# Performance work log

Hardware: AMD Instinct MI355X
Metric: run time of the kernel (lower is better)

Reference implementation:

```python
import jax, jax.numpy as jnp
import numpy as np

EPS = 1e-7
CP_NUM = 16
P_NUM_TOTAL = 1024
P_PER_SEG = P_NUM_TOTAL // CP_NUM  # 64, matches int(p_num / cp_num)
ALPHA = 0.5


def setup_inputs() -> dict:
    key = jax.random.key(0)
    cps = jax.random.normal(key, (16384, CP_NUM, 2), dtype=jnp.float32)
    return {"cps": cps}


def reference(cps):
    # Centripetal Catmull-Rom spline sampling (closed curve), fully vectorized
    # over segments and sample points instead of the original double Python loop.
    B, S, D = cps.shape  # S == cp_num
    P = P_PER_SEG

    # Close the curve: append first control point.  [B, S+1, D]
    cc = jnp.concatenate([cps, cps[:, :1, :]], axis=1)

    # Boundary extension lengths (detached in the original via .detach_()).
    l01 = jax.lax.stop_gradient(
        jnp.sqrt(jnp.sum((cc[:, 0] - cc[:, 1]) ** 2, axis=-1) + EPS))[:, None]
    llast = jax.lax.stop_gradient(
        jnp.sqrt(jnp.sum((cc[:, -1] - cc[:, -2]) ** 2, axis=-1) + EPS))[:, None]
    aux_first = cc[:, 0] - l01 / llast * (cc[:, -1] - cc[:, -2])
    aux_last = cc[:, -1] + llast / l01 * (cc[:, 1] - cc[:, 0])
    # Auxiliary control points. [B, S+3, D]
    aux = jnp.concatenate([aux_first[:, None], cc, aux_last[:, None]], axis=1)

    # Centripetal knot vector: t[i] = t[i-1] + ||aux_i - aux_{i-1}||^alpha (detached).
    seg_len = jnp.sqrt(jnp.sum((aux[:, 1:] - aux[:, :-1]) ** 2, axis=-1)) ** ALPHA
    t = jnp.concatenate(
        [jnp.zeros((B, 1), dtype=cps.dtype), jnp.cumsum(seg_len, axis=1)], axis=1)
    t = jax.lax.stop_gradient(t)  # [B, S+3]

    idx = jnp.arange(S)
    # Knot windows per segment, broadcast to [B, S, 1, 1].
    t0 = t[:, idx][:, :, None, None]
    t1 = t[:, idx + 1][:, :, None, None]
    t2 = t[:, idx + 2][:, :, None, None]
    t3 = t[:, idx + 3][:, :, None, None]
    # Control point windows per segment, broadcast to [B, S, 1, D].
    P0 = aux[:, idx][:, :, None, :]
    P1 = aux[:, idx + 1][:, :, None, :]
    P2 = aux[:, idx + 2][:, :, None, :]
    P3 = aux[:, idx + 3][:, :, None, :]

    # batch_linspace(t1, t2, P): P points inclusive of both endpoints. [B,S,P,1]
    u = jnp.linspace(0.0, 1.0, P, dtype=cps.dtype)[None, None, :, None]
    tv = t1 + (t2 - t1) * u

    # Barry-Goldman pyramid of weighted blends.
    x01 = (t1 - tv) / (t1 - t0) * P0 + (tv - t0) / (t1 - t0) * P1
    x12 = (t2 - tv) / (t2 - t1) * P1 + (tv - t1) / (t2 - t1) * P2
    x23 = (t3 - tv) / (t3 - t2) * P2 + (tv - t2) / (t3 - t2) * P3
    x012 = (t2 - tv) / (t2 - t0) * x01 + (tv - t0) / (t2 - t0) * x12
    x123 = (t3 - tv) / (t3 - t1) * x12 + (tv - t1) / (t3 - t1) * x23
    pts = (t2 - tv) / (t2 - t1) * x012 + (tv - t1) / (t2 - t1) * x123  # [B,S,P,D]

    return pts.reshape(B, S * P, D)
```

## Files before the change

kernel.cpp:

```cpp
#include <hip/hip_runtime.h>

#define CP_NUM 16
#define SEGS   16
#define WPB    4
#define BLK    (WPB * 64)

typedef float f32x4 __attribute__((ext_vector_type(4)));

__device__ __forceinline__ float frcp(float x) { return __builtin_amdgcn_rcpf(x); }

__global__ __launch_bounds__(BLK, 8) void spline_poly_kernel(
    const float* __restrict__ cps, float* __restrict__ out, int nb)
{
    __shared__ __align__(16) float s_cp [WPB][CP_NUM * 2];
    __shared__ __align__(16) float s_aux[WPB][19 * 2];
    __shared__ __align__(16) float s_t  [WPB][20];
    __shared__ __align__(16) float s_seg[WPB][SEGS][12];

    const int lane = threadIdx.x & 63;
    const int wv   = threadIdx.x >> 6;
    const int b    = blockIdx.x * WPB + wv;
    if (b >= nb) return;

    if (lane < 8) {
        reinterpret_cast<float4*>(s_cp[wv])[lane] =
            reinterpret_cast<const float4*>(cps + (size_t)b * (CP_NUM * 2))[lane];
    }
    __builtin_amdgcn_wave_barrier();

    if (lane < 19) {
        const float c0x = s_cp[wv][0],  c0y = s_cp[wv][1];
        const float c1x = s_cp[wv][2],  c1y = s_cp[wv][3];
        const float cLx = s_cp[wv][30], cLy = s_cp[wv][31];
        const float dx01 = c0x - c1x, dy01 = c0y - c1y;
        const float l01   = sqrtf(dx01 * dx01 + dy01 * dy01 + 1e-7f);
        const float dxl = c0x - cLx, dyl = c0y - cLy;
        const float llast = sqrtf(dxl * dxl + dyl * dyl + 1e-7f);
        float ax, ay;
        if (lane == 0) {
            const float r = l01 * frcp(llast);
            ax = c0x - r * dxl;  ay = c0y - r * dyl;
        } else if (lane <= CP_NUM) {
            ax = s_cp[wv][(lane - 1) * 2];  ay = s_cp[wv][(lane - 1) * 2 + 1];
        } else if (lane == CP_NUM + 1) {
            ax = c0x;  ay = c0y;
        } else {
            const float r = llast * frcp(l01);
            ax = c0x + r * (c1x - c0x);  ay = c0y + r * (c1y - c0y);
        }
        s_aux[wv][lane * 2]     = ax;
        s_aux[wv][lane * 2 + 1] = ay;
    }
    __builtin_amdgcn_wave_barrier();

    float len = 0.f;
    if (lane < 18) {
        const float dx = s_aux[wv][(lane + 1) * 2]     - s_aux[wv][lane * 2];
        const float dy = s_aux[wv][(lane + 1) * 2 + 1] - s_aux[wv][lane * 2 + 1];
        len = sqrtf(sqrtf(dx * dx + dy * dy));
    }
    #pragma unroll
    for (int d = 1; d < 32; d <<= 1) {
        const float n = __shfl_up(len, d);
        if (lane >= d) len += n;
    }
    if (lane == 0) s_t[wv][0] = 0.f;
    if (lane < 18) s_t[wv][lane + 1] = len;
    __builtin_amdgcn_wave_barrier();

    if (lane < SEGS) {
        const float t0 = s_t[wv][lane];
        const float t1 = s_t[wv][lane + 1];
        const float t2 = s_t[wv][lane + 2];
        const float t3 = s_t[wv][lane + 3];
        const float A  = t1 - t0, Bk = t2 - t1, C = t3 - t2;
        const float BC = Bk + C;
        const float r10 = frcp(A);
        const float r21 = frcp(Bk);
        const float r32 = frcp(C);
        const float r20 = frcp(A + Bk);
        const float r31 = frcp(BC);

        float* sp = s_seg[wv][lane];
        #pragma unroll
        for (int d = 0; d < 2; ++d) {
            const float P0 = s_aux[wv][lane * 2 + d];
            const float P1 = s_aux[wv][lane * 2 + 2 + d];
            const float P2 = s_aux[wv][lane * 2 + 4 + d];
            const float P3 = s_aux[wv][lane * 2 + 6 + d];
            const float L1c0 = P1,                        L1c1 = (P1 - P0) * r10;
            const float L2c0 = P1,                        L2c1 = (P2 - P1) * r21;
            const float L3c0 = (BC * P2 - Bk * P3) * r32, L3c1 = (P3 - P2) * r32;
            const float Q1c0 = r20 * (Bk * L1c0 + A * L2c0);
            const float Q1c1 = r20 * (Bk * L1c1 - L1c0 + A * L2c1 + L2c0);
            const float Q1c2 = r20 * (L2c1 - L1c1);
            const float Q2c0 = r31 * (BC * L2c0);
            const float Q2c1 = r31 * (BC * L2c1 - L2c0 + L3c0);
            const float Q2c2 = r31 * (L3c1 - L2c1);
            sp[d * 4 + 0] = Q1c0;
            sp[d * 4 + 1] = Q1c1 + r21 * (Q2c0 - Q1c0);
            sp[d * 4 + 2] = Q1c2 + r21 * (Q2c1 - Q1c1);
            sp[d * 4 + 3] = r21 * (Q2c2 - Q1c2);
        }
        sp[8] = Bk;
    }
    __builtin_amdgcn_wave_barrier();

    f32x4* outw = reinterpret_cast<f32x4*>(out + (size_t)b * (SEGS * 64 * 2));
    const int   hi = lane >> 5;
    const float q0 = (float)((lane & 31) * 2)     * (1.f / 63.f);
    const float q1 = (float)((lane & 31) * 2 + 1) * (1.f / 63.f);
    #pragma unroll
    for (int i = 0; i < 8; ++i) {
        const float* sp = s_seg[wv][2 * i + hi];
        const f32x4 cx = *reinterpret_cast<const f32x4*>(sp);
        const f32x4 cy = *reinterpret_cast<const f32x4*>(sp + 4);
        const float dt = sp[8];
        const float s0 = dt * q0;
        const float s1 = dt * q1;
        f32x4 o;
        o.x = ((cx.w * s0 + cx.z) * s0 + cx.y) * s0 + cx.x;
        o.y = ((cy.w * s0 + cy.z) * s0 + cy.y) * s0 + cy.x;
        o.z = ((cx.w * s1 + cx.z) * s1 + cx.y) * s1 + cx.x;
        o.w = ((cy.w * s1 + cy.z) * s1 + cy.y) * s1 + cy.x;
        outw[lane + 64 * i] = o;
    }
}

extern "C" void kernel_launch(void* const* d_in, const int* in_sizes, int n_in,
                              void* d_out, int out_size, void* d_ws, size_t ws_size,
                              hipStream_t stream) {
    const float* cps = (const float*)d_in[0];
    float* out = (float*)d_out;
    const int B = in_sizes[0] / (CP_NUM * 2);
    const int grid = (B + WPB - 1) / WPB;
    spline_poly_kernel<<<grid, BLK, 0, stream>>>(cps, out, B);
}
```

Baseline: 27.88 us.

## Process two curves per wavefront using half-wave setup lanes

Each wavefront now handles two batch items. Each 32-lane half computes the auxiliary points, the knot prefix sum (via 32-wide shuffles) and the segment polynomial coefficients for one curve, then the whole wave writes both curves' outputs. The goal is to fill the mostly idle lanes in the serial setup phase and halve the grid size, trading that for a longer output loop per wave and less parallelism across waves.

```diff
diff --git a/kernel.cpp b/kernel.cpp
--- a/kernel.cpp
+++ b/kernel.cpp
@@ -12,67 +12,73 @@
 __global__ __launch_bounds__(BLK, 8) void spline_poly_kernel(
     const float* __restrict__ cps, float* __restrict__ out, int nb)
 {
-    __shared__ __align__(16) float s_cp [WPB][CP_NUM * 2];
-    __shared__ __align__(16) float s_aux[WPB][19 * 2];
-    __shared__ __align__(16) float s_t  [WPB][20];
-    __shared__ __align__(16) float s_seg[WPB][SEGS][12];
+    __shared__ __align__(16) float4 s_cp [WPB][16];
+    __shared__ __align__(16) float  s_aux[WPB][2][19 * 2];
+    __shared__ __align__(16) float  s_t  [WPB][2][20];
+    __shared__ __align__(16) float  s_seg[WPB][2][SEGS][12];
 
     const int lane = threadIdx.x & 63;
     const int wv   = threadIdx.x >> 6;
-    const int b    = blockIdx.x * WPB + wv;
-    if (b >= nb) return;
+    const int half = lane >> 5;
+    const int r    = lane & 31;
+    const int pw   = blockIdx.x * WPB + wv;
+    const int base = pw * 2;
+    if (base >= nb) return;
+    const int ncur = (nb - base < 2) ? (nb - base) : 2;
 
-    if (lane < 8) {
-        reinterpret_cast<float4*>(s_cp[wv])[lane] =
-            reinterpret_cast<const float4*>(cps + (size_t)b * (CP_NUM * 2))[lane];
+    if (lane < 8 * ncur) {
+        s_cp[wv][lane] =
+            reinterpret_cast<const float4*>(cps + (size_t)base * (CP_NUM * 2))[lane];
     }
     __builtin_amdgcn_wave_barrier();
 
-    if (lane < 19) {
-        const float c0x = s_cp[wv][0],  c0y = s_cp[wv][1];
-        const float c1x = s_cp[wv][2],  c1y = s_cp[wv][3];
-        const float cLx = s_cp[wv][30], cLy = s_cp[wv][31];
+    const float* cpw = reinterpret_cast<const float*>(s_cp[wv]) + half * 32;
+
+    if (r < 19) {
+        const float c0x = cpw[0],  c0y = cpw[1];
+        const float c1x = cpw[2],  c1y = cpw[3];
+        const float cLx = cpw[30], cLy = cpw[31];
         const float dx01 = c0x - c1x, dy01 = c0y - c1y;
         const float l01   = sqrtf(dx01 * dx01 + dy01 * dy01 + 1e-7f);
         const float dxl = c0x - cLx, dyl = c0y - cLy;
         const float llast = sqrtf(dxl * dxl + dyl * dyl + 1e-7f);
         float ax, ay;
-        if (lane == 0) {
-            const float r = l01 * frcp(llast);
-            ax = c0x - r * dxl;  ay = c0y - r * dyl;
-        } else if (lane <= CP_NUM) {
-            ax = s_cp[wv][(lane - 1) * 2];  ay = s_cp[wv][(lane - 1) * 2 + 1];
-        } else if (lane == CP_NUM + 1) {
+        if (r == 0) {
+            const float rr = l01 * frcp(llast);
+            ax = c0x - rr * dxl;  ay = c0y - rr * dyl;
+        } else if (r <= CP_NUM) {
+            ax = cpw[(r - 1) * 2];  ay = cpw[(r - 1) * 2 + 1];
+        } else if (r == CP_NUM + 1) {
             ax = c0x;  ay = c0y;
         } else {
-            const float r = llast * frcp(l01);
-            ax = c0x + r * (c1x - c0x);  ay = c0y + r * (c1y - c0y);
+            const float rr = llast * frcp(l01);
+            ax = c0x + rr * (c1x - c0x);  ay = c0y + rr * (c1y - c0y);
         }
-        s_aux[wv][lane * 2]     = ax;
-        s_aux[wv][lane * 2 + 1] = ay;
+        s_aux[wv][half][r * 2]     = ax;
+        s_aux[wv][half][r * 2 + 1] = ay;
     }
     __builtin_amdgcn_wave_barrier();
 
     float len = 0.f;
-    if (lane < 18) {
-        const float dx = s_aux[wv][(lane + 1) * 2]     - s_aux[wv][lane * 2];
-        const float dy = s_aux[wv][(lane + 1) * 2 + 1] - s_aux[wv][lane * 2 + 1];
+    if (r < 18) {
+        const float dx = s_aux[wv][half][(r + 1) * 2]     - s_aux[wv][half][r * 2];
+        const float dy = s_aux[wv][half][(r + 1) * 2 + 1] - s_aux[wv][half][r * 2 + 1];
         len = sqrtf(sqrtf(dx * dx + dy * dy));
     }
     #pragma unroll
     for (int d = 1; d < 32; d <<= 1) {
-        const float n = __shfl_up(len, d);
-        if (lane >= d) len += n;
+        const float n = __shfl_up(len, d, 32);
+        if (r >= d) len += n;
     }
-    if (lane == 0) s_t[wv][0] = 0.f;
-    if (lane < 18) s_t[wv][lane + 1] = len;
+    if (r == 0) s_t[wv][half][0] = 0.f;
+    if (r < 18) s_t[wv][half][r + 1] = len;
     __builtin_amdgcn_wave_barrier();
 
-    if (lane < SEGS) {
-        const float t0 = s_t[wv][lane];
-        const float t1 = s_t[wv][lane + 1];
-        const float t2 = s_t[wv][lane + 2];
-        const float t3 = s_t[wv][lane + 3];
+    if (r < SEGS) {
+        const float t0 = s_t[wv][half][r];
+        const float t1 = s_t[wv][half][r + 1];
+        const float t2 = s_t[wv][half][r + 2];
+        const float t3 = s_t[wv][half][r + 3];
         const float A  = t1 - t0, Bk = t2 - t1, C = t3 - t2;
         const float BC = Bk + C;
         const float r10 = frcp(A);
@@ -81,13 +87,13 @@
         const float r20 = frcp(A + Bk);
         const float r31 = frcp(BC);
 
-        float* sp = s_seg[wv][lane];
+        float* sp = s_seg[wv][half][r];
         #pragma unroll
         for (int d = 0; d < 2; ++d) {
-            const float P0 = s_aux[wv][lane * 2 + d];
-            const float P1 = s_aux[wv][lane * 2 + 2 + d];
-            const float P2 = s_aux[wv][lane * 2 + 4 + d];
-            const float P3 = s_aux[wv][lane * 2 + 6 + d];
+            const float P0 = s_aux[wv][half][r * 2 + d];
+            const float P1 = s_aux[wv][half][r * 2 + 2 + d];
+            const float P2 = s_aux[wv][half][r * 2 + 4 + d];
+            const float P3 = s_aux[wv][half][r * 2 + 6 + d];
             const float L1c0 = P1,                        L1c1 = (P1 - P0) * r10;
             const float L2c0 = P1,                        L2c1 = (P2 - P1) * r21;
             const float L3c0 = (BC * P2 - Bk * P3) * r32, L3c1 = (P3 - P2) * r32;
@@ -106,24 +112,27 @@
     }
     __builtin_amdgcn_wave_barrier();
 
-    f32x4* outw = reinterpret_cast<f32x4*>(out + (size_t)b * (SEGS * 64 * 2));
-    const int   hi = lane >> 5;
-    const float q0 = (float)((lane & 31) * 2)     * (1.f / 63.f);
-    const float q1 = (float)((lane & 31) * 2 + 1) * (1.f / 63.f);
+    const float q0 = (float)(r * 2)     * (1.f / 63.f);
+    const float q1 = (float)(r * 2 + 1) * (1.f / 63.f);
     #pragma unroll
-    for (int i = 0; i < 8; ++i) {
-        const float* sp = s_seg[wv][2 * i + hi];
-        const f32x4 cx = *reinterpret_cast<const f32x4*>(sp);
-        const f32x4 cy = *reinterpret_cast<const f32x4*>(sp + 4);
-        const float dt = sp[8];
-        const float s0 = dt * q0;
-        const float s1 = dt * q1;
-        f32x4 o;
-        o.x = ((cx.w * s0 + cx.z) * s0 + cx.y) * s0 + cx.x;
-        o.y = ((cy.w * s0 + cy.z) * s0 + cy.y) * s0 + cy.x;
-        o.z = ((cx.w * s1 + cx.z) * s1 + cx.y) * s1 + cx.x;
-        o.w = ((cy.w * s1 + cy.z) * s1 + cy.y) * s1 + cy.x;
-        outw[lane + 64 * i] = o;
+    for (int cv = 0; cv < 2; ++cv) {
+        if (base + cv >= nb) break;
+        f32x4* outw = reinterpret_cast<f32x4*>(out + (size_t)(base + cv) * (SEGS * 64 * 2));
+        #pragma unroll
+        for (int j = 0; j < 8; ++j) {
+            const float* sp = s_seg[wv][cv][2 * j + half];
+            const f32x4 cx = *reinterpret_cast<const f32x4*>(sp);
+            const f32x4 cy = *reinterpret_cast<const f32x4*>(sp + 4);
+            const float dt = sp[8];
+            const float s0 = dt * q0;
+            const float s1 = dt * q1;
+            f32x4 o;
+            o.x = ((cx.w * s0 + cx.z) * s0 + cx.y) * s0 + cx.x;
+            o.y = ((cy.w * s0 + cy.z) * s0 + cy.y) * s0 + cy.x;
+            o.z = ((cx.w * s1 + cx.z) * s1 + cx.y) * s1 + cx.x;
+            o.w = ((cy.w * s1 + cy.z) * s1 + cy.y) * s1 + cy.x;
+            outw[lane + 64 * j] = o;
+        }
     }
 }
 
@@ -133,6 +142,7 @@
     const float* cps = (const float*)d_in[0];
     float* out = (float*)d_out;
     const int B = in_sizes[0] / (CP_NUM * 2);
-    const int grid = (B + WPB - 1) / WPB;
+    const int npairs = (B + 1) / 2;
+    const int grid = (npairs + WPB - 1) / WPB;
     spline_poly_kernel<<<grid, BLK, 0, stream>>>(cps, out, B);
 }
```

Measured after the change: 27.96 us. About the same (+0.3%).
